# Kernel optimization log

Hardware: AMD Instinct MI355X
Metric: run time of the kernel (lower is better)

Reference implementation:

```python
import jax, jax.numpy as jnp
import numpy as np

N, F, H, C, B = 50000, 128, 128, 32, 512
E = 600000


def _norm_edges(edge_index, n):
    # PyG GCNConv default: add self-loops, symmetric normalization
    src = jnp.concatenate([edge_index[0], jnp.arange(n, dtype=edge_index.dtype)])
    dst = jnp.concatenate([edge_index[1], jnp.arange(n, dtype=edge_index.dtype)])
    deg = jax.ops.segment_sum(jnp.ones_like(dst, dtype=jnp.float32), dst, num_segments=n)
    inv_sqrt = jnp.where(deg > 0, jax.lax.rsqrt(jnp.maximum(deg, 1.0)), 0.0)
    norm = inv_sqrt[src] * inv_sqrt[dst]  # [E+N]
    return src, dst, norm


def _gcn_conv(x, W, b, src, dst, norm, n):
    h = x @ W                                  # [N, H] dense transform
    msg = norm[:, None] * h[src]               # gather + per-edge scale
    out = jax.ops.segment_sum(msg, dst, num_segments=n)  # scatter-add
    return out + b


def setup_inputs() -> dict:
    key = jax.random.key(0)
    ks = jax.random.split(key, 20)
    x = jax.random.normal(ks[0], (N, F), dtype=jnp.float32)
    edge_index = jax.random.randint(ks[1], (2, E), 0, N, dtype=jnp.int64)
    batch = jnp.sort(jax.random.randint(ks[2], (N,), 0, B, dtype=jnp.int64))
    d = {"x": x, "edge_index": edge_index, "batch": batch}
    dims_in = [F, H, H, H, H, H]
    for i in range(6):
        s = 1.0 / np.sqrt(dims_in[i])
        d[f"W{i+1}"] = jax.random.uniform(ks[3 + i], (dims_in[i], H), jnp.float32, -s, s)
        d[f"b{i+1}"] = jnp.zeros((H,), jnp.float32)
    s = 1.0 / np.sqrt(H)
    d["lin_W"] = jax.random.uniform(ks[10], (H, C), jnp.float32, -s, s)
    d["lin_b"] = jnp.zeros((C,), jnp.float32)
    return d


def reference(x, edge_index, batch, W1, b1, W2, b2, W3, b3, W4, b4, W5, b5, W6, b6, lin_W, lin_b):
    n = x.shape[0]
    src, dst, norm = _norm_edges(edge_index, n)
    Ws = [W1, W2, W3, W4, W5, W6]
    bs = [b1, b2, b3, b4, b5, b6]
    h = x
    for i in range(6):
        h = _gcn_conv(h, Ws[i], bs[i], src, dst, norm, n)
        if i < 5:
            h = jax.nn.relu(h)
    # global mean pool over graph ids
    counts = jax.ops.segment_sum(jnp.ones((n,), jnp.float32), batch, num_segments=B)
    pooled = jax.ops.segment_sum(h, batch, num_segments=B) / jnp.maximum(counts, 1.0)[:, None]
    # dropout is identity in eval mode
    return pooled @ lin_W + lin_b
```

## Files before the change

### kernel.cpp

```cpp
#include <hip/hip_runtime.h>
#include <hip/hip_fp16.h>


static inline int ceil_div(int a, int b) { return (a + b - 1) / b; }

typedef _Float16 f16x8 __attribute__((ext_vector_type(8)));
typedef _Float16 f16x4 __attribute__((ext_vector_type(4)));
typedef float f32x4 __attribute__((ext_vector_type(4)));


__global__ __launch_bounds__(256) void hist_i32(const int* __restrict__ idx,
                                                int* __restrict__ cnt, int n) {
  int i = blockIdx.x * 256 + threadIdx.x;
  if (i < n) atomicAdd(&cnt[idx[i]], 1);
}

__global__ __launch_bounds__(256) void scanA(const int* __restrict__ deg,
                                             int* __restrict__ tmp,
                                             int* __restrict__ sums,
                                             float* __restrict__ inv, int n) {
  __shared__ int s[256];
  int t = threadIdx.x;
  int gid = blockIdx.x * 256 + t;
  int d = (gid < n) ? deg[gid] : 0;
  if (gid < n) inv[gid] = rsqrtf((float)(d + 1));
  s[t] = d;
  __syncthreads();
  for (int off = 1; off < 256; off <<= 1) {
    int add = (t >= off) ? s[t - off] : 0;
    __syncthreads();
    s[t] += add;
    __syncthreads();
  }
  if (gid < n) tmp[gid] = s[t];
  if (t == 255) sums[blockIdx.x] = s[255];
}

__global__ __launch_bounds__(256) void scanB(int* __restrict__ sums, int nchunk) {
  __shared__ int s[256];
  int t = threadIdx.x;
  s[t] = (t < nchunk) ? sums[t] : 0;
  __syncthreads();
  for (int off = 1; off < 256; off <<= 1) {
    int add = (t >= off) ? s[t - off] : 0;
    __syncthreads();
    s[t] += add;
    __syncthreads();
  }
  if (t < nchunk) sums[t] = s[t];
}

__global__ __launch_bounds__(256) void scanC(const int* __restrict__ tmp,
                                             const int* __restrict__ sums,
                                             const int* __restrict__ deg,
                                             int* __restrict__ rp,
                                             int* __restrict__ cursor, int n) {
  int gid = blockIdx.x * 256 + threadIdx.x;
  if (gid < n) {
    int off = (blockIdx.x > 0) ? sums[blockIdx.x - 1] : 0;
    int incl = tmp[gid] + off;
    rp[gid + 1] = incl;
    cursor[gid] = incl - deg[gid];
    if (gid == 0) rp[0] = 0;
  }
}

__global__ __launch_bounds__(256) void scatter_edges(const int* __restrict__ src,
                                                     const int* __restrict__ dst,
                                                     int* __restrict__ cursor,
                                                     int* __restrict__ col, int E) {
  int i = blockIdx.x * 256 + threadIdx.x;
  if (i < E) {
    int d = dst[i];
    int pos = atomicAdd(&cursor[d], 1);
    col[pos] = src[i];
  }
}

struct WP { const float* p[6]; };
__global__ __launch_bounds__(256) void setup_fuse(const float* __restrict__ x,
                                                  _Float16* __restrict__ h16,
                                                  WP wp, _Float16* __restrict__ wt,
                                                  const int* __restrict__ batch,
                                                  int* __restrict__ gstart,
                                                  int nelem, int nodes, int B,
                                                  int nbF) {
  int blk = blockIdx.x;
  if (blk < nbF) {
    int i = (blk * 256 + threadIdx.x) * 4;
    if (i < nelem) {
      float4 v = *(const float4*)&x[i];
      f16x4 o = {(_Float16)v.x, (_Float16)v.y, (_Float16)v.z, (_Float16)v.w};
      *(f16x4*)&h16[i] = o;
    }
  } else if (blk < nbF + 384) {
    int b2 = blk - nbF;
    int wi = b2 >> 6;
    int e = (b2 & 63) * 256 + threadIdx.x;
    int k = e >> 7, c = e & 127;
    wt[((size_t)wi << 14) + (size_t)c * 128 + k] = (_Float16)wp.p[wi][e];
  } else {
    int g = (blk - nbF - 384) * 256 + threadIdx.x;
    if (g <= B) {
      int lo = 0, hi = nodes;
      while (lo < hi) {
        int mid = (lo + hi) >> 1;
        if (batch[mid] < g) lo = mid + 1; else hi = mid;
      }
      gstart[g] = lo;
    }
  }
}


__global__ __launch_bounds__(256, 2) void gemm_mfma_p(const _Float16* __restrict__ A,
                                                      const _Float16* __restrict__ Wt,
                                                      const float* __restrict__ inv,
                                                      _Float16* __restrict__ out,
                                                      int nrows) {
  int lane = threadIdx.x & 63;
  int wv = threadIdx.x >> 6;
  int r = lane & 15, g = lane >> 4;

  f16x8 b[8][4];
  const _Float16* bp = Wt + (size_t)r * 128 + g * 8;
#pragma unroll
  for (int ct = 0; ct < 8; ++ct) {
    const _Float16* bt = bp + (size_t)ct * 16 * 128;
#pragma unroll
    for (int ks = 0; ks < 4; ++ks) b[ct][ks] = *(const f16x8*)(bt + ks * 32);
  }

  int tiles = (nrows + 15) >> 4;
  int nwaves = (int)gridDim.x * 4;
  for (int tt = blockIdx.x * 4 + wv; tt < tiles; tt += nwaves) {
    int rowBase = tt * 16;

    int arow = rowBase + r;
    if (arow >= nrows) arow = nrows - 1;
    const _Float16* ap = A + (size_t)arow * 128 + g * 8;
    f16x8 a0 = *(const f16x8*)(ap + 0);
    f16x8 a1 = *(const f16x8*)(ap + 32);
    f16x8 a2 = *(const f16x8*)(ap + 64);
    f16x8 a3 = *(const f16x8*)(ap + 96);

    f32x4 acc[8];
#pragma unroll
    for (int ct = 0; ct < 8; ++ct) acc[ct] = (f32x4){0.f, 0.f, 0.f, 0.f};

#pragma unroll
    for (int ct = 0; ct < 8; ++ct) {
      acc[ct] = __builtin_amdgcn_mfma_f32_16x16x32_f16(b[ct][0], a0, acc[ct], 0, 0, 0);
      acc[ct] = __builtin_amdgcn_mfma_f32_16x16x32_f16(b[ct][1], a1, acc[ct], 0, 0, 0);
      acc[ct] = __builtin_amdgcn_mfma_f32_16x16x32_f16(b[ct][2], a2, acc[ct], 0, 0, 0);
      acc[ct] = __builtin_amdgcn_mfma_f32_16x16x32_f16(b[ct][3], a3, acc[ct], 0, 0, 0);
    }

    int node = rowBase + r;
    if (node < nrows) {
      float iv = inv[node];
      _Float16* op = out + (size_t)node * 128 + g * 4;
#pragma unroll
      for (int ct = 0; ct < 8; ++ct) {
        __half2 lo = __floats2half2_rn(acc[ct][0] * iv, acc[ct][1] * iv);
        __half2 hi = __floats2half2_rn(acc[ct][2] * iv, acc[ct][3] * iv);
        uint2 sv;
        sv.x = *(unsigned*)&lo;
        sv.y = *(unsigned*)&hi;
        *(uint2*)(op + ct * 16) = sv;
      }
    }
  }
}

__global__ __launch_bounds__(256) void aggregate(const __half* __restrict__ hs,
                                                 const int* __restrict__ col,
                                                 const int* __restrict__ rp,
                                                 const float* __restrict__ inv,
                                                 const float* __restrict__ bias,
                                                 __half* __restrict__ out, int n,
                                                 int dorelu) {
  int node = blockIdx.x * 4 + (threadIdx.x >> 6);
  if (node >= n) return;
  int lane = threadIdx.x & 63;
  const __half2* h2 = (const __half2*)hs;

  int beg = rp[node], end = rp[node + 1];
  float2 self = __half22float2(h2[(size_t)node * 64 + lane]);
  float sx[8], sy[8];
  sx[0] = self.x; sy[0] = self.y;
#pragma unroll
  for (int i = 1; i < 8; ++i) { sx[i] = 0.f; sy[i] = 0.f; }

  int e = beg;
  for (; e + 8 <= end; e += 8) {
    int idx[8];
#pragma unroll
    for (int i = 0; i < 8; ++i) idx[i] = col[e + i];
    __half2 v[8];
#pragma unroll
    for (int i = 0; i < 8; ++i) v[i] = h2[(size_t)idx[i] * 64 + lane];
#pragma unroll
    for (int i = 0; i < 8; ++i) {
      float2 f = __half22float2(v[i]);
      sx[i] += f.x; sy[i] += f.y;
    }
  }
  if (e + 4 <= end) {
    int idx[4];
#pragma unroll
    for (int i = 0; i < 4; ++i) idx[i] = col[e + i];
    __half2 v[4];
#pragma unroll
    for (int i = 0; i < 4; ++i) v[i] = h2[(size_t)idx[i] * 64 + lane];
#pragma unroll
    for (int i = 0; i < 4; ++i) {
      float2 f = __half22float2(v[i]);
      sx[i] += f.x; sy[i] += f.y;
    }
    e += 4;
  }
  for (; e < end; ++e) {
    int s = col[e];
    float2 f = __half22float2(h2[(size_t)s * 64 + lane]);
    sx[0] += f.x; sy[0] += f.y;
  }

  float ax = (sx[0] + sx[1]) + (sx[2] + sx[3]);
  float bx = (sx[4] + sx[5]) + (sx[6] + sx[7]);
  float ay = (sy[0] + sy[1]) + (sy[2] + sy[3]);
  float by = (sy[4] + sy[5]) + (sy[6] + sy[7]);

  float iv = inv[node];
  float rx = iv * (ax + bx) + bias[lane * 2 + 0];
  float ry = iv * (ay + by) + bias[lane * 2 + 1];
  if (dorelu) { rx = fmaxf(rx, 0.f); ry = fmaxf(ry, 0.f); }
  ((__half2*)out)[(size_t)node * 64 + lane] = __floats2half2_rn(rx, ry);
}

__global__ __launch_bounds__(128) void pool_mean(const __half* __restrict__ h,
                                                 const int* __restrict__ gstart,
                                                 float* __restrict__ pooled) {
  int g = blockIdx.x;
  int c = threadIdx.x;
  int s = gstart[g], e = gstart[g + 1];
  float acc = 0.f;
  for (int v = s; v < e; ++v) acc += __half2float(h[(size_t)v * 128 + c]);
  int cnt = e - s;
  pooled[(size_t)g * 128 + c] = acc / (float)(cnt > 0 ? cnt : 1);
}

__global__ __launch_bounds__(256) void final_lin(const float* __restrict__ pooled,
                                                 const float* __restrict__ lw,
                                                 const float* __restrict__ lb,
                                                 float* __restrict__ out, int total) {
  int idx = blockIdx.x * 256 + threadIdx.x;
  if (idx >= total) return;
  int g = idx >> 5;
  int c = idx & 31;
  float s = 0.f;
#pragma unroll 8
  for (int k = 0; k < 128; ++k) s += pooled[(size_t)g * 128 + k] * lw[k * 32 + c];
  out[idx] = s + lb[c];
}


extern "C" void kernel_launch(void* const* d_in, const int* in_sizes, int n_in,
                              void* d_out, int out_size, void* d_ws, size_t ws_size,
                              hipStream_t stream) {
  const float* x = (const float*)d_in[0];
  const int* ei = (const int*)d_in[1];
  const int* batch = (const int*)d_in[2];
  WP wp;
  const float* bvec[6];
  for (int i = 0; i < 6; ++i) {
    wp.p[i] = (const float*)d_in[3 + 2 * i];
    bvec[i] = (const float*)d_in[4 + 2 * i];
  }
  const float* linW = (const float*)d_in[15];
  const float* linb = (const float*)d_in[16];
  float* out = (float*)d_out;

  const int F = 128, H = 128, C = 32;
  const int N = in_sizes[0] / F;
  const int E = in_sizes[1] / 2;
  const int B = out_size / C;
  const int* src = ei;
  const int* dst = ei + E;

  char* w = (char*)d_ws;
  auto alloc = [&](size_t bytes) -> char* {
    char* p = w;
    w += (bytes + 255) & ~(size_t)255;
    return p;
  };
  int* deg = (int*)alloc((size_t)N * 4);
  float* inv = (float*)alloc((size_t)N * 4);
  int* tmp = (int*)alloc((size_t)N * 4);
  int* sums = (int*)alloc(256 * 4);
  int* rp = (int*)alloc((size_t)(N + 1) * 4);
  int* cursor = (int*)alloc((size_t)N * 4);
  int* col = (int*)alloc((size_t)E * 4);
  int* gstart = (int*)alloc((size_t)(B + 1) * 4);
  _Float16* h16 = (_Float16*)alloc((size_t)N * H * 2);
  _Float16* hs16 = (_Float16*)alloc((size_t)N * H * 2);
  _Float16* wt16 = (_Float16*)alloc((size_t)6 * H * H * 2);
  float* pooled = (float*)alloc((size_t)B * H * 4);
  (void)n_in; (void)ws_size;

  hipMemsetAsync(deg, 0, (size_t)N * 4, stream);

  hist_i32<<<ceil_div(E, 256), 256, 0, stream>>>(dst, deg, E);

  int nchunk = ceil_div(N, 256);
  scanA<<<nchunk, 256, 0, stream>>>(deg, tmp, sums, inv, N);
  scanB<<<1, 256, 0, stream>>>(sums, nchunk);
  scanC<<<nchunk, 256, 0, stream>>>(tmp, sums, deg, rp, cursor, N);

  int nbF = ceil_div(N * F / 4, 256);
  int nbBS = ceil_div(B + 1, 256);
  setup_fuse<<<nbF + 384 + nbBS, 256, 0, stream>>>(x, h16, wp, wt16, batch, gstart,
                                                   N * F, N, B, nbF);

  scatter_edges<<<ceil_div(E, 256), 256, 0, stream>>>(src, dst, cursor, col, E);

  for (int l = 0; l < 6; ++l) {
    gemm_mfma_p<<<512, 256, 0, stream>>>(h16, wt16 + ((size_t)l << 14), inv, hs16, N);
    aggregate<<<ceil_div(N, 4), 256, 0, stream>>>((const __half*)hs16, col, rp, inv,
                                                  bvec[l], (__half*)h16, N,
                                                  (l < 5) ? 1 : 0);
  }

  pool_mean<<<B, 128, 0, stream>>>((const __half*)h16, gstart, pooled);
  final_lin<<<ceil_div(B * C, 256), 256, 0, stream>>>(pooled, linW, linb, out, B * C);
}
```

Measured before the change: 493.3 us.

## Gather 4 neighbors per wavefront with 16-byte vector loads in aggregate

The aggregation kernel now splits each 64-lane wavefront into four 16-lane groups. Each group handles a different neighbor edge and each lane loads 8 fp16 values (16 bytes) rather than one half2. Partial sums are combined with cross-lane shuffles at the end, and the first group writes a vectorized 16-byte output with bias and ReLU. The aim is fewer, wider memory transactions and more independent edge gathers in flight per wavefront, at the cost of shuffle reductions and idle lanes in the final write and tail.

```diff
diff --git a/kernel.cpp b/kernel.cpp
--- a/kernel.cpp
+++ b/kernel.cpp
@@ -173,69 +173,88 @@
   }
 }
 
-__global__ __launch_bounds__(256) void aggregate(const __half* __restrict__ hs,
+__global__ __launch_bounds__(256) void aggregate(const _Float16* __restrict__ hs,
                                                  const int* __restrict__ col,
                                                  const int* __restrict__ rp,
                                                  const float* __restrict__ inv,
                                                  const float* __restrict__ bias,
-                                                 __half* __restrict__ out, int n,
+                                                 _Float16* __restrict__ out, int n,
                                                  int dorelu) {
   int node = blockIdx.x * 4 + (threadIdx.x >> 6);
   if (node >= n) return;
   int lane = threadIdx.x & 63;
-  const __half2* h2 = (const __half2*)hs;
+  int sub = lane >> 4;
+  int cl = lane & 15;
 
   int beg = rp[node], end = rp[node + 1];
-  float2 self = __half22float2(h2[(size_t)node * 64 + lane]);
-  float sx[8], sy[8];
-  sx[0] = self.x; sy[0] = self.y;
-#pragma unroll
-  for (int i = 1; i < 8; ++i) { sx[i] = 0.f; sy[i] = 0.f; }
+  float acc[8];
+#pragma unroll
+  for (int j = 0; j < 8; ++j) acc[j] = 0.f;
+
+  if (sub == 0) {
+    f16x8 v = *(const f16x8*)(hs + (size_t)node * 128 + cl * 8);
+#pragma unroll
+    for (int j = 0; j < 8; ++j) acc[j] += (float)v[j];
+  }
 
   int e = beg;
-  for (; e + 8 <= end; e += 8) {
-    int idx[8];
-#pragma unroll
-    for (int i = 0; i < 8; ++i) idx[i] = col[e + i];
-    __half2 v[8];
-#pragma unroll
-    for (int i = 0; i < 8; ++i) v[i] = h2[(size_t)idx[i] * 64 + lane];
-#pragma unroll
-    for (int i = 0; i < 8; ++i) {
-      float2 f = __half22float2(v[i]);
-      sx[i] += f.x; sy[i] += f.y;
-    }
+  for (; e + 16 <= end; e += 16) {
+    int i0 = col[e + sub];
+    int i1 = col[e + 4 + sub];
+    int i2 = col[e + 8 + sub];
+    int i3 = col[e + 12 + sub];
+    f16x8 v0 = *(const f16x8*)(hs + (size_t)i0 * 128 + cl * 8);
+    f16x8 v1 = *(const f16x8*)(hs + (size_t)i1 * 128 + cl * 8);
+    f16x8 v2 = *(const f16x8*)(hs + (size_t)i2 * 128 + cl * 8);
+    f16x8 v3 = *(const f16x8*)(hs + (size_t)i3 * 128 + cl * 8);
+#pragma unroll
+    for (int j = 0; j < 8; ++j)
+      acc[j] += ((float)v0[j] + (float)v1[j]) + ((float)v2[j] + (float)v3[j]);
+  }
+  if (e + 8 <= end) {
+    int i0 = col[e + sub];
+    int i1 = col[e + 4 + sub];
+    f16x8 v0 = *(const f16x8*)(hs + (size_t)i0 * 128 + cl * 8);
+    f16x8 v1 = *(const f16x8*)(hs + (size_t)i1 * 128 + cl * 8);
+#pragma unroll
+    for (int j = 0; j < 8; ++j) acc[j] += (float)v0[j] + (float)v1[j];
+    e += 8;
   }
   if (e + 4 <= end) {
-    int idx[4];
-#pragma unroll
-    for (int i = 0; i < 4; ++i) idx[i] = col[e + i];
-    __half2 v[4];
-#pragma unroll
-    for (int i = 0; i < 4; ++i) v[i] = h2[(size_t)idx[i] * 64 + lane];
-#pragma unroll
-    for (int i = 0; i < 4; ++i) {
-      float2 f = __half22float2(v[i]);
-      sx[i] += f.x; sy[i] += f.y;
-    }
+    int i0 = col[e + sub];
+    f16x8 v0 = *(const f16x8*)(hs + (size_t)i0 * 128 + cl * 8);
+#pragma unroll
+    for (int j = 0; j < 8; ++j) acc[j] += (float)v0[j];
     e += 4;
   }
-  for (; e < end; ++e) {
-    int s = col[e];
-    float2 f = __half22float2(h2[(size_t)s * 64 + lane]);
-    sx[0] += f.x; sy[0] += f.y;
-  }
-
-  float ax = (sx[0] + sx[1]) + (sx[2] + sx[3]);
-  float bx = (sx[4] + sx[5]) + (sx[6] + sx[7]);
-  float ay = (sy[0] + sy[1]) + (sy[2] + sy[3]);
-  float by = (sy[4] + sy[5]) + (sy[6] + sy[7]);
-
-  float iv = inv[node];
-  float rx = iv * (ax + bx) + bias[lane * 2 + 0];
-  float ry = iv * (ay + by) + bias[lane * 2 + 1];
-  if (dorelu) { rx = fmaxf(rx, 0.f); ry = fmaxf(ry, 0.f); }
-  ((__half2*)out)[(size_t)node * 64 + lane] = __floats2half2_rn(rx, ry);
+  int rem = end - e;
+  if (sub < rem) {
+    int i0 = col[e + sub];
+    f16x8 v0 = *(const f16x8*)(hs + (size_t)i0 * 128 + cl * 8);
+#pragma unroll
+    for (int j = 0; j < 8; ++j) acc[j] += (float)v0[j];
+  }
+
+#pragma unroll
+  for (int j = 0; j < 8; ++j) {
+    acc[j] += __shfl_xor(acc[j], 16, 64);
+    acc[j] += __shfl_xor(acc[j], 32, 64);
+  }
+
+  if (sub == 0) {
+    float iv = inv[node];
+    float4 b0 = *(const float4*)&bias[cl * 8];
+    float4 b1 = *(const float4*)&bias[cl * 8 + 4];
+    float rb[8] = {b0.x, b0.y, b0.z, b0.w, b1.x, b1.y, b1.z, b1.w};
+    f16x8 o;
+#pragma unroll
+    for (int j = 0; j < 8; ++j) {
+      float r = iv * acc[j] + rb[j];
+      if (dorelu) r = fmaxf(r, 0.f);
+      o[j] = (_Float16)r;
+    }
+    *(f16x8*)(out + (size_t)node * 128 + cl * 8) = o;
+  }
 }
 
 __global__ __launch_bounds__(128) void pool_mean(const __half* __restrict__ h,
@@ -326,9 +345,8 @@
 
   for (int l = 0; l < 6; ++l) {
     gemm_mfma_p<<<512, 256, 0, stream>>>(h16, wt16 + ((size_t)l << 14), inv, hs16, N);
-    aggregate<<<ceil_div(N, 4), 256, 0, stream>>>((const __half*)hs16, col, rp, inv,
-                                                  bvec[l], (__half*)h16, N,
-                                                  (l < 5) ? 1 : 0);
+    aggregate<<<ceil_div(N, 4), 256, 0, stream>>>(hs16, col, rp, inv, bvec[l],
+                                                  h16, N, (l < 5) ? 1 : 0);
   }
 
   pool_mean<<<B, 128, 0, stream>>>((const __half*)h16, gstart, pooled);
```

New measurement: 484.7 us. No clear change (-1.8%).

## Fuse neighbor aggregation and MFMA GEMM into one per-layer kernel

Applied to the files above, without the earlier changes.

Uses (A·X)W = A(XW) to fuse each layer into a single kernel. Each wave gathers neighbor features for 16 nodes into LDS, then runs the MFMA GEMM on that aggregated tile and applies the normalization, bias and ReLU in the epilogue. Activations are stored pre-scaled by inv-sqrt-degree, so the input conversion also applies that scale. This removes the intermediate hs16 write and read and one launch per layer. The cost is that the latency-bound gather now runs inside a register-heavy kernel with far fewer waves in flight and only 4-way ILP per node, so gather latency may be poorly hidden.

```diff
diff --git a/kernel.cpp b/kernel.cpp
--- a/kernel.cpp
+++ b/kernel.cpp
@@ -6,6 +6,7 @@
 
 typedef _Float16 f16x8 __attribute__((ext_vector_type(8)));
 typedef _Float16 f16x4 __attribute__((ext_vector_type(4)));
+typedef _Float16 f16x2 __attribute__((ext_vector_type(2)));
 typedef float f32x4 __attribute__((ext_vector_type(4)));
 
 
@@ -79,7 +80,8 @@
 
 struct WP { const float* p[6]; };
 __global__ __launch_bounds__(256) void setup_fuse(const float* __restrict__ x,
-                                                  _Float16* __restrict__ h16,
+                                                  const float* __restrict__ inv,
+                                                  _Float16* __restrict__ hp,
                                                   WP wp, _Float16* __restrict__ wt,
                                                   const int* __restrict__ batch,
                                                   int* __restrict__ gstart,
@@ -89,9 +91,11 @@
   if (blk < nbF) {
     int i = (blk * 256 + threadIdx.x) * 4;
     if (i < nelem) {
+      float iv = inv[i >> 7];
       float4 v = *(const float4*)&x[i];
-      f16x4 o = {(_Float16)v.x, (_Float16)v.y, (_Float16)v.z, (_Float16)v.w};
-      *(f16x4*)&h16[i] = o;
+      f16x4 o = {(_Float16)(v.x * iv), (_Float16)(v.y * iv),
+                 (_Float16)(v.z * iv), (_Float16)(v.w * iv)};
+      *(f16x4*)&hp[i] = o;
     }
   } else if (blk < nbF + 384) {
     int b2 = blk - nbF;
@@ -113,11 +117,12 @@
 }
 
 
-__global__ __launch_bounds__(256, 2) void gemm_mfma_p(const _Float16* __restrict__ A,
-                                                      const _Float16* __restrict__ Wt,
-                                                      const float* __restrict__ inv,
-                                                      _Float16* __restrict__ out,
-                                                      int nrows) {
+__global__ __launch_bounds__(256, 2) void layer_fused(
+    const _Float16* __restrict__ hp, const _Float16* __restrict__ Wt,
+    const float* __restrict__ inv, const int* __restrict__ col,
+    const int* __restrict__ rp, const float* __restrict__ bias,
+    _Float16* __restrict__ out, int n, int dorelu) {
+  __shared__ float ms[4][16][132];
   int lane = threadIdx.x & 63;
   int wv = threadIdx.x >> 6;
   int r = lane & 15, g = lane >> 4;
@@ -126,44 +131,79 @@
   const _Float16* bp = Wt + (size_t)r * 128 + g * 8;
 #pragma unroll
   for (int ct = 0; ct < 8; ++ct) {
-    const _Float16* bt = bp + (size_t)ct * 16 * 128;
-#pragma unroll
-    for (int ks = 0; ks < 4; ++ks) b[ct][ks] = *(const f16x8*)(bt + ks * 32);
-  }
-
-  int tiles = (nrows + 15) >> 4;
+#pragma unroll
+    for (int ks = 0; ks < 4; ++ks)
+      b[ct][ks] = *(const f16x8*)(bp + ct * 2048 + ks * 32);
+  }
+
+  const f16x2* hp2 = (const f16x2*)hp;
+  int ngroups = (n + 15) >> 4;
   int nwaves = (int)gridDim.x * 4;
-  for (int tt = blockIdx.x * 4 + wv; tt < tiles; tt += nwaves) {
-    int rowBase = tt * 16;
-
-    int arow = rowBase + r;
-    if (arow >= nrows) arow = nrows - 1;
-    const _Float16* ap = A + (size_t)arow * 128 + g * 8;
-    f16x8 a0 = *(const f16x8*)(ap + 0);
-    f16x8 a1 = *(const f16x8*)(ap + 32);
-    f16x8 a2 = *(const f16x8*)(ap + 64);
-    f16x8 a3 = *(const f16x8*)(ap + 96);
+
+  for (int grp = blockIdx.x * 4 + wv; grp < ngroups; grp += nwaves) {
+    int base = grp << 4;
+
+    for (int j = 0; j < 16; ++j) {
+      int node = base + j;
+      float ax = 0.f, ay = 0.f, bx = 0.f, by = 0.f;
+      float cx = 0.f, cy = 0.f, dx = 0.f, dy = 0.f;
+      if (node < n) {
+        int beg = rp[node], end = rp[node + 1];
+        f16x2 sv = hp2[(size_t)node * 64 + lane];
+        ax = (float)sv[0]; ay = (float)sv[1];
+        int e = beg;
+        for (; e + 4 <= end; e += 4) {
+          int i0 = col[e + 0], i1 = col[e + 1], i2 = col[e + 2], i3 = col[e + 3];
+          f16x2 v0 = hp2[(size_t)i0 * 64 + lane];
+          f16x2 v1 = hp2[(size_t)i1 * 64 + lane];
+          f16x2 v2 = hp2[(size_t)i2 * 64 + lane];
+          f16x2 v3 = hp2[(size_t)i3 * 64 + lane];
+          ax += (float)v0[0]; ay += (float)v0[1];
+          bx += (float)v1[0]; by += (float)v1[1];
+          cx += (float)v2[0]; cy += (float)v2[1];
+          dx += (float)v3[0]; dy += (float)v3[1];
+        }
+        for (; e < end; ++e) {
+          f16x2 v = hp2[(size_t)col[e] * 64 + lane];
+          ax += (float)v[0]; ay += (float)v[1];
+        }
+      }
+      *(float2*)&ms[wv][j][2 * lane] =
+          make_float2((ax + bx) + (cx + dx), (ay + by) + (cy + dy));
+    }
 
     f32x4 acc[8];
 #pragma unroll
     for (int ct = 0; ct < 8; ++ct) acc[ct] = (f32x4){0.f, 0.f, 0.f, 0.f};
 
 #pragma unroll
-    for (int ct = 0; ct < 8; ++ct) {
-      acc[ct] = __builtin_amdgcn_mfma_f32_16x16x32_f16(b[ct][0], a0, acc[ct], 0, 0, 0);
-      acc[ct] = __builtin_amdgcn_mfma_f32_16x16x32_f16(b[ct][1], a1, acc[ct], 0, 0, 0);
-      acc[ct] = __builtin_amdgcn_mfma_f32_16x16x32_f16(b[ct][2], a2, acc[ct], 0, 0, 0);
-      acc[ct] = __builtin_amdgcn_mfma_f32_16x16x32_f16(b[ct][3], a3, acc[ct], 0, 0, 0);
-    }
-
-    int node = rowBase + r;
-    if (node < nrows) {
+    for (int ks = 0; ks < 4; ++ks) {
+      const float* mrow = &ms[wv][r][ks * 32 + g * 8];
+      f16x8 a;
+#pragma unroll
+      for (int kk = 0; kk < 8; ++kk) a[kk] = (_Float16)mrow[kk];
+#pragma unroll
+      for (int ct = 0; ct < 8; ++ct)
+        acc[ct] = __builtin_amdgcn_mfma_f32_16x16x32_f16(b[ct][ks], a, acc[ct], 0, 0, 0);
+    }
+
+    int node = base + r;
+    if (node < n) {
       float iv = inv[node];
       _Float16* op = out + (size_t)node * 128 + g * 4;
 #pragma unroll
       for (int ct = 0; ct < 8; ++ct) {
-        __half2 lo = __floats2half2_rn(acc[ct][0] * iv, acc[ct][1] * iv);
-        __half2 hi = __floats2half2_rn(acc[ct][2] * iv, acc[ct][3] * iv);
+        const float4 bb = *(const float4*)&bias[ct * 16 + g * 4];
+        float r0 = iv * acc[ct][0] + bb.x;
+        float r1 = iv * acc[ct][1] + bb.y;
+        float r2 = iv * acc[ct][2] + bb.z;
+        float r3 = iv * acc[ct][3] + bb.w;
+        if (dorelu) {
+          r0 = iv * fmaxf(r0, 0.f); r1 = iv * fmaxf(r1, 0.f);
+          r2 = iv * fmaxf(r2, 0.f); r3 = iv * fmaxf(r3, 0.f);
+        }
+        __half2 lo = __floats2half2_rn(r0, r1);
+        __half2 hi = __floats2half2_rn(r2, r3);
         uint2 sv;
         sv.x = *(unsigned*)&lo;
         sv.y = *(unsigned*)&hi;
@@ -171,71 +211,6 @@
       }
     }
   }
-}
-
-__global__ __launch_bounds__(256) void aggregate(const __half* __restrict__ hs,
-                                                 const int* __restrict__ col,
-                                                 const int* __restrict__ rp,
-                                                 const float* __restrict__ inv,
-                                                 const float* __restrict__ bias,
-                                                 __half* __restrict__ out, int n,
-                                                 int dorelu) {
-  int node = blockIdx.x * 4 + (threadIdx.x >> 6);
-  if (node >= n) return;
-  int lane = threadIdx.x & 63;
-  const __half2* h2 = (const __half2*)hs;
-
-  int beg = rp[node], end = rp[node + 1];
-  float2 self = __half22float2(h2[(size_t)node * 64 + lane]);
-  float sx[8], sy[8];
-  sx[0] = self.x; sy[0] = self.y;
-#pragma unroll
-  for (int i = 1; i < 8; ++i) { sx[i] = 0.f; sy[i] = 0.f; }
-
-  int e = beg;
-  for (; e + 8 <= end; e += 8) {
-    int idx[8];
-#pragma unroll
-    for (int i = 0; i < 8; ++i) idx[i] = col[e + i];
-    __half2 v[8];
-#pragma unroll
-    for (int i = 0; i < 8; ++i) v[i] = h2[(size_t)idx[i] * 64 + lane];
-#pragma unroll
-    for (int i = 0; i < 8; ++i) {
-      float2 f = __half22float2(v[i]);
-      sx[i] += f.x; sy[i] += f.y;
-    }
-  }
-  if (e + 4 <= end) {
-    int idx[4];
-#pragma unroll
-    for (int i = 0; i < 4; ++i) idx[i] = col[e + i];
-    __half2 v[4];
-#pragma unroll
-    for (int i = 0; i < 4; ++i) v[i] = h2[(size_t)idx[i] * 64 + lane];
-#pragma unroll
-    for (int i = 0; i < 4; ++i) {
-      float2 f = __half22float2(v[i]);
-      sx[i] += f.x; sy[i] += f.y;
-    }
-    e += 4;
-  }
-  for (; e < end; ++e) {
-    int s = col[e];
-    float2 f = __half22float2(h2[(size_t)s * 64 + lane]);
-    sx[0] += f.x; sy[0] += f.y;
-  }
-
-  float ax = (sx[0] + sx[1]) + (sx[2] + sx[3]);
-  float bx = (sx[4] + sx[5]) + (sx[6] + sx[7]);
-  float ay = (sy[0] + sy[1]) + (sy[2] + sy[3]);
-  float by = (sy[4] + sy[5]) + (sy[6] + sy[7]);
-
-  float iv = inv[node];
-  float rx = iv * (ax + bx) + bias[lane * 2 + 0];
-  float ry = iv * (ay + by) + bias[lane * 2 + 1];
-  if (dorelu) { rx = fmaxf(rx, 0.f); ry = fmaxf(ry, 0.f); }
-  ((__half2*)out)[(size_t)node * 64 + lane] = __floats2half2_rn(rx, ry);
 }
 
 __global__ __launch_bounds__(128) void pool_mean(const __half* __restrict__ h,
@@ -302,8 +277,8 @@
   int* cursor = (int*)alloc((size_t)N * 4);
   int* col = (int*)alloc((size_t)E * 4);
   int* gstart = (int*)alloc((size_t)(B + 1) * 4);
-  _Float16* h16 = (_Float16*)alloc((size_t)N * H * 2);
-  _Float16* hs16 = (_Float16*)alloc((size_t)N * H * 2);
+  _Float16* h16a = (_Float16*)alloc((size_t)N * H * 2);
+  _Float16* h16b = (_Float16*)alloc((size_t)N * H * 2);
   _Float16* wt16 = (_Float16*)alloc((size_t)6 * H * H * 2);
   float* pooled = (float*)alloc((size_t)B * H * 4);
   (void)n_in; (void)ws_size;
@@ -319,18 +294,19 @@
 
   int nbF = ceil_div(N * F / 4, 256);
   int nbBS = ceil_div(B + 1, 256);
-  setup_fuse<<<nbF + 384 + nbBS, 256, 0, stream>>>(x, h16, wp, wt16, batch, gstart,
-                                                   N * F, N, B, nbF);
+  setup_fuse<<<nbF + 384 + nbBS, 256, 0, stream>>>(x, inv, h16a, wp, wt16, batch,
+                                                   gstart, N * F, N, B, nbF);
 
   scatter_edges<<<ceil_div(E, 256), 256, 0, stream>>>(src, dst, cursor, col, E);
 
+  _Float16* cur = h16a;
+  _Float16* nxt = h16b;
   for (int l = 0; l < 6; ++l) {
-    gemm_mfma_p<<<512, 256, 0, stream>>>(h16, wt16 + ((size_t)l << 14), inv, hs16, N);
-    aggregate<<<ceil_div(N, 4), 256, 0, stream>>>((const __half*)hs16, col, rp, inv,
-                                                  bvec[l], (__half*)h16, N,
-                                                  (l < 5) ? 1 : 0);
-  }
-
-  pool_mean<<<B, 128, 0, stream>>>((const __half*)h16, gstart, pooled);
+    layer_fused<<<512, 256, 0, stream>>>(cur, wt16 + ((size_t)l << 14), inv, col, rp,
+                                         bvec[l], nxt, N, (l < 5) ? 1 : 0);
+    _Float16* t = cur; cur = nxt; nxt = t;
+  }
+
+  pool_mean<<<B, 128, 0, stream>>>((const __half*)cur, gstart, pooled);
   final_lin<<<ceil_div(B * C, 256), 256, 0, stream>>>(pooled, linW, linb, out, B * C);
 }
```

New measurement: 844.9 us. 1.71x slower.
